# Performance work log

Measured on AMD Instinct MI355X. Metric: run time of the kernel, lower is better.

The kernel has to match this reference:

```python
import jax, jax.numpy as jnp
import numpy as np

B, H, W, T, D = 8, 32, 32, 4, 768
BLK = 4  # super-block of base tokens used to generate the static partition


def _build_descs():
    """Deterministic partition: 4x4 blocks of the 32x32 grid, scale = block_idx % 3."""
    d0, d1, d2 = [], [], []
    for t in range(T):
        i = 0
        for by in range(0, H, BLK):
            for bx in range(0, W, BLK):
                s = i % 3
                i += 1
                if s == 0:  # 16 base (scale-0) tokens
                    for yy in range(by, by + BLK):
                        for xx in range(bx, bx + BLK):
                            d0.append((yy, xx, t))
                elif s == 1:  # four 2x2 (scale-1) tokens
                    for yy in range(by, by + BLK, 2):
                        for xx in range(bx, bx + BLK, 2):
                            d1.append((yy, xx, t))
                else:  # one 4x4 (scale-2) token
                    d2.append((by, bx, t))
    return (jnp.asarray(np.array(d0, dtype=np.int32)),
            jnp.asarray(np.array(d1, dtype=np.int32)),
            jnp.asarray(np.array(d2, dtype=np.int32)))


def setup_inputs() -> dict:
    key = jax.random.key(0)
    ks = jax.random.split(key, 8)
    base = jax.random.normal(ks[0], (B, H, W, T, D), dtype=jnp.float32)
    desc0, desc1, desc2 = _build_descs()  # [1408,3], [336,3], [84,3] of (y, x, t)
    ws = 0.05  # keep conv outputs O(1)
    w1 = jax.random.normal(ks[1], (D, D, 2, 2), jnp.float32) * ws
    b1 = jax.random.normal(ks[2], (D,), jnp.float32) * ws
    w2a = jax.random.normal(ks[3], (D, D, 2, 2), jnp.float32) * ws
    b2a = jax.random.normal(ks[4], (D,), jnp.float32) * ws
    w2b = jax.random.normal(ks[5], (D, D, 2, 2), jnp.float32) * ws
    b2b = jax.random.normal(ks[6], (D,), jnp.float32) * ws
    return {"base_patch_embeddings": base, "desc0": desc0, "desc1": desc1,
            "desc2": desc2, "w1": w1, "b1": b1, "w2a": w2a, "b2a": b2a,
            "w2b": w2b, "b2b": b2b}


def _gather_blocks(base, desc, S):
    """Gather [B, N, S, S, D] blocks at (y, x, t) descriptors."""
    off = jnp.arange(S)
    ys = desc[:, 0][:, None, None] + off[None, :, None]  # [N,S,1]
    xs = desc[:, 1][:, None, None] + off[None, None, :]  # [N,1,S]
    ts = desc[:, 2][:, None, None]                       # [N,1,1]
    return base[:, ys, xs, ts, :]                        # [B,N,S,S,D]


def _down(x, w, b):
    """One k=2, s=2 conv over grouped blocks: [B,N,S,S,D] -> [B,N,S/2,S/2,D]."""
    Bn, N, S, _, Dd = x.shape
    x = x.reshape(Bn, N, S // 2, 2, S // 2, 2, Dd)
    return jnp.einsum('bnhiwjc,dcij->bnhwd', x, w) + b


def reference(base_patch_embeddings, desc0, desc1, desc2, w1, b1, w2a, b2a, w2b, b2b):
    base = base_patch_embeddings
    # scale 0: direct gather of base tokens
    tok0 = base[:, desc0[:, 0], desc0[:, 1], desc0[:, 2], :]          # [B,N0,D]
    # scale 1: 2x2 blocks -> one conv
    blk1 = _gather_blocks(base, desc1, 2)                             # [B,N1,2,2,D]
    tok1 = _down(blk1, w1, b1)[:, :, 0, 0, :]                         # [B,N1,D]
    # scale 2: 4x4 blocks -> two convs
    blk2 = _gather_blocks(base, desc2, 4)                             # [B,N2,4,4,D]
    tok2 = _down(_down(blk2, w2a, b2a), w2b, b2b)[:, :, 0, 0, :]      # [B,N2,D]
    tokens = jnp.concatenate([tok0, tok1, tok2], axis=1)              # [B,1828,D]
    # positions: (y, x, size_in_base, timestep)
    def _pos(desc, size):
        n = desc.shape[0]
        return jnp.concatenate([desc[:, :2],
                                jnp.full((n, 1), size, jnp.int32),
                                desc[:, 2:3]], axis=1)
    positions = jnp.concatenate([_pos(desc0, 1), _pos(desc1, 2), _pos(desc2, 4)], axis=0)
    return tokens, positions
```

## Files before the change

### kernel.cpp

```cpp
#include <hip/hip_runtime.h>
#include <cstdint>
#include <cstddef>

#define BB    8
#define HH    32
#define WW    32
#define TT    4
#define DD    768
#define N0    1408
#define N1    336
#define N2    84
#define NTOK  1828
#define TOK_FLOATS (BB*NTOK*DD)
#define KDIM  3072
#define M1    (BB*N1)
#define M2A   (BB*N2*4)
#define M2B   (BB*N2)

typedef __attribute__((ext_vector_type(8))) short          short8v;
typedef __attribute__((ext_vector_type(8))) unsigned short us8;
typedef __attribute__((ext_vector_type(4))) float          f32x4;

__device__ __forceinline__ unsigned short f2bf(float f) {
    unsigned int u = __float_as_uint(f);
    u += 0x7fffu + ((u >> 16) & 1u);
    return (unsigned short)(u >> 16);
}

__global__ __launch_bounds__(256) void positions_kernel(
    const int* __restrict__ d0, const int* __restrict__ d1,
    const int* __restrict__ d2, float* __restrict__ pos)
{
    int n = blockIdx.x * 256 + threadIdx.x;
    if (n >= NTOK) return;
    int y, x, t, s;
    if (n < N0)           { y = d0[n*3];         x = d0[n*3+1];         t = d0[n*3+2];         s = 1; }
    else if (n < N0+N1)   { int m = n - N0;      y = d1[m*3]; x = d1[m*3+1]; t = d1[m*3+2];    s = 2; }
    else                  { int m = n - N0 - N1; y = d2[m*3]; x = d2[m*3+1]; t = d2[m*3+2];    s = 4; }
    pos[n*4+0] = (float)y; pos[n*4+1] = (float)x; pos[n*4+2] = (float)s; pos[n*4+3] = (float)t;
}

__global__ __launch_bounds__(256) void gather0_kernel(
    const float* __restrict__ base, const int* __restrict__ d0,
    float* __restrict__ out)
{
    const int total = BB * N0 * (DD/4);
    for (int idx = blockIdx.x * 256 + threadIdx.x; idx < total; idx += gridDim.x * 256) {
        int d4 = idx % (DD/4);
        int nb = idx / (DD/4);
        int n  = nb % N0;
        int b  = nb / N0;
        int y = d0[n*3], x = d0[n*3+1], t = d0[n*3+2];
        const float4* src = (const float4*)(base + (size_t)(((b*HH + y)*WW + x)*TT + t) * DD) + d4;
        float4*       dst = (float4*)(out + ((size_t)b*NTOK + n) * DD) + d4;
        *dst = *src;
    }
}

__global__ __launch_bounds__(256) void castW_kernel(
    const float* __restrict__ wA, unsigned short* __restrict__ oA,
    const float* __restrict__ wB, unsigned short* __restrict__ oB,
    const float* __restrict__ wC, unsigned short* __restrict__ oC)
{
    const float* w; unsigned short* Wtb;
    if      (blockIdx.z == 0) { w = wA; Wtb = oA; }
    else if (blockIdx.z == 1) { w = wB; Wtb = oB; }
    else                      { w = wC; Wtb = oC; }
    int idx = blockIdx.x * 256 + threadIdx.x;
    int n = idx / KDIM;
    int r = idx - n * KDIM;
    int p = r / DD;
    int c = r - p * DD;
    Wtb[idx] = f2bf(w[n*KDIM + c*4 + p]);
}

__global__ __launch_bounds__(256) void gatherA_kernel(
    const float* __restrict__ base, const int* __restrict__ d1,
    const int* __restrict__ d2, unsigned short* __restrict__ A1,
    unsigned short* __restrict__ A2, int half)
{
    int idx = blockIdx.x * 256 + threadIdx.x;
    int rm = idx / 384;
    int o  = idx - rm * 384;
    if (half == 2) rm += M1;
    int k0 = o * 8;
    int p  = k0 / DD, c0 = k0 - p * DD;
    const float* rowp;
    unsigned short* dst;
    if (rm < M1) {
        int m = rm, b = m / N1, tok = m - b * N1;
        int y = d1[tok*3] + (p>>1), x = d1[tok*3+1] + (p&1), t = d1[tok*3+2];
        rowp = base + (size_t)(((b*HH + y)*WW + x)*TT + t) * DD;
        dst  = A1 + (size_t)m * KDIM + k0;
    } else {
        int m = rm - M1, b = m / (N2*4), r = m - b * (N2*4);
        int n = r >> 2, hw = r & 3, h = hw >> 1, w = hw & 1;
        int y = d2[n*3] + 2*h + (p>>1), x = d2[n*3+1] + 2*w + (p&1), t = d2[n*3+2];
        rowp = base + (size_t)(((b*HH + y)*WW + x)*TT + t) * DD;
        dst  = A2 + (size_t)m * KDIM + k0;
    }
    float4 v0 = *(const float4*)(rowp + c0);
    float4 v1 = *(const float4*)(rowp + c0 + 4);
    us8 r8;
    r8[0]=f2bf(v0.x); r8[1]=f2bf(v0.y); r8[2]=f2bf(v0.z); r8[3]=f2bf(v0.w);
    r8[4]=f2bf(v1.x); r8[5]=f2bf(v1.y); r8[6]=f2bf(v1.z); r8[7]=f2bf(v1.w);
    *(us8*)dst = r8;
}

struct GCfg {
    const unsigned short* A;
    const unsigned short* Bw;
    const float*          bias;
    float*                outf;
    unsigned short*       outb;
    int                   M;
    int                   mode;
};

__global__ __launch_bounds__(256) void mfma_gemm_kernel(GCfg c0, GCfg c1)
{
    GCfg cfg = (blockIdx.z == 0) ? c0 : c1;
    constexpr int LDT = 72;
    __shared__ unsigned short As[64  * LDT];
    __shared__ unsigned short Bs[128 * LDT];

    const int tid  = threadIdx.x;
    const int lane = tid & 63;
    const int wv   = tid >> 6;
    const int wr   = wv >> 1, wc = wv & 1;
    const int m0   = blockIdx.x * 64, n0 = blockIdx.y * 128;

    const int ar = tid >> 2, aci = (tid & 3) * 2;
    const int br = tid >> 1, bci = (tid & 1) * 4;
    int mrow = m0 + ar; if (mrow >= cfg.M) mrow = cfg.M - 1;
    const unsigned short* aptr = cfg.A  + (size_t)mrow    * KDIM + aci * 8;
    const unsigned short* bptr = cfg.Bw + (size_t)(n0+br) * KDIM + bci * 8;

    f32x4 acc[2][4];
    #pragma unroll
    for (int i = 0; i < 2; ++i)
        #pragma unroll
        for (int j = 0; j < 4; ++j)
            #pragma unroll
            for (int r = 0; r < 4; ++r) acc[i][j][r] = 0.f;

    us8 a0, a1, b0, b1, b2, b3;
    a0 = *(const us8*)(aptr);      a1 = *(const us8*)(aptr + 8);
    b0 = *(const us8*)(bptr);      b1 = *(const us8*)(bptr + 8);
    b2 = *(const us8*)(bptr + 16); b3 = *(const us8*)(bptr + 24);

    for (int k0 = 0; k0 < KDIM; k0 += 64) {
        __syncthreads();
        *(us8*)&As[ar*LDT +  aci   *8] = a0;
        *(us8*)&As[ar*LDT + (aci+1)*8] = a1;
        *(us8*)&Bs[br*LDT +  bci   *8] = b0;
        *(us8*)&Bs[br*LDT + (bci+1)*8] = b1;
        *(us8*)&Bs[br*LDT + (bci+2)*8] = b2;
        *(us8*)&Bs[br*LDT + (bci+3)*8] = b3;
        __syncthreads();
        if (k0 + 64 < KDIM) {
            const unsigned short* ap = aptr + k0 + 64;
            const unsigned short* bp = bptr + k0 + 64;
            a0 = *(const us8*)(ap);      a1 = *(const us8*)(ap + 8);
            b0 = *(const us8*)(bp);      b1 = *(const us8*)(bp + 8);
            b2 = *(const us8*)(bp + 16); b3 = *(const us8*)(bp + 24);
        }
        #pragma unroll
        for (int ks = 0; ks < 2; ++ks) {
            short8v av[2], bv[4];
            #pragma unroll
            for (int fm = 0; fm < 2; ++fm) {
                int row = wr*32 + fm*16 + (lane & 15);
                av[fm] = *(const short8v*)&As[row*LDT + (ks*4 + (lane>>4))*8];
            }
            #pragma unroll
            for (int fn = 0; fn < 4; ++fn) {
                int row = wc*64 + fn*16 + (lane & 15);
                bv[fn] = *(const short8v*)&Bs[row*LDT + (ks*4 + (lane>>4))*8];
            }
            #pragma unroll
            for (int fm = 0; fm < 2; ++fm)
                #pragma unroll
                for (int fn = 0; fn < 4; ++fn)
                    acc[fm][fn] = __builtin_amdgcn_mfma_f32_16x16x32_bf16(
                        av[fm], bv[fn], acc[fm][fn], 0, 0, 0);
        }
    }

    const int rg = lane >> 4, col = lane & 15;
    const int mode = cfg.mode;
    #pragma unroll
    for (int fm = 0; fm < 2; ++fm) {
        #pragma unroll
        for (int fn = 0; fn < 4; ++fn) {
            int n = n0 + wc*64 + fn*16 + col;
            float bs = cfg.bias[n];
            #pragma unroll
            for (int r = 0; r < 4; ++r) {
                int m = m0 + wr*32 + fm*16 + rg*4 + r;
                if (m >= cfg.M) continue;
                float v = acc[fm][fn][r] + bs;
                if (mode == 0) {
                    int b = m / N1, tok = m - b*N1;
                    cfg.outf[((size_t)b*NTOK + N0 + tok)*DD + n] = v;
                } else if (mode == 1) {
                    cfg.outb[(size_t)m*DD + n] = f2bf(v);
                } else {
                    int b = m / N2, tk = m - b*N2;
                    cfg.outf[((size_t)b*NTOK + N0 + N1 + tk)*DD + n] = v;
                }
            }
        }
    }
}

extern "C" void kernel_launch(void* const* d_in, const int* in_sizes, int n_in,
                              void* d_out, int out_size, void* d_ws, size_t ws_size,
                              hipStream_t stream)
{
    const float* base  = (const float*)d_in[0];
    const int*   desc0 = (const int*)  d_in[1];
    const int*   desc1 = (const int*)  d_in[2];
    const int*   desc2 = (const int*)  d_in[3];
    const float* w1    = (const float*)d_in[4];
    const float* b1    = (const float*)d_in[5];
    const float* w2a   = (const float*)d_in[6];
    const float* b2a   = (const float*)d_in[7];
    const float* w2b   = (const float*)d_in[8];
    const float* b2b   = (const float*)d_in[9];

    float* out = (float*)d_out;
    float* pos = (float*)d_out + TOK_FLOATS;
    unsigned short* ws = (unsigned short*)d_ws;

    positions_kernel<<<8, 256, 0, stream>>>(desc0, desc1, desc2, pos);
    gather0_kernel<<<2048, 256, 0, stream>>>(base, desc0, out);

    const size_t ABF = (size_t)M1 * KDIM;
    const size_t WTB = (size_t)DD * KDIM;
    const size_t Y1  = (size_t)M2A * DD;
    const size_t need_full = (2*ABF + Y1 + 3*WTB) * sizeof(unsigned short);

    if (ws_size >= need_full) {
        unsigned short* A1  = ws;
        unsigned short* A2  = A1  + ABF;
        unsigned short* y1b = A2  + ABF;
        unsigned short* W1  = y1b + Y1;
        unsigned short* W2a = W1  + WTB;
        unsigned short* W2b = W2a + WTB;
        castW_kernel<<<dim3(9216, 1, 3), 256, 0, stream>>>(w1, W1, w2a, W2a, w2b, W2b);
        gatherA_kernel<<<8064, 256, 0, stream>>>(base, desc1, desc2, A1, A2, 0);
        GCfg cA = { A1, W1,  b1,  out,     nullptr, M1,  0 };
        GCfg cB = { A2, W2a, b2a, nullptr, y1b,     M2A, 1 };
        mfma_gemm_kernel<<<dim3(42, 6, 2), 256, 0, stream>>>(cA, cB);
        GCfg cC = { y1b, W2b, b2b, out, nullptr, M2B, 2 };
        mfma_gemm_kernel<<<dim3(11, 6, 1), 256, 0, stream>>>(cC, cC);
    } else {
        unsigned short* A1  = ws;
        unsigned short* Wt  = A1 + ABF;
        unsigned short* y1b = Wt + WTB;
        castW_kernel<<<dim3(9216, 1, 1), 256, 0, stream>>>(w1, Wt, w1, Wt, w1, Wt);
        gatherA_kernel<<<4032, 256, 0, stream>>>(base, desc1, desc2, A1, A1, 1);
        GCfg cA = { A1, Wt, b1, out, nullptr, M1, 0 };
        mfma_gemm_kernel<<<dim3(42, 6, 1), 256, 0, stream>>>(cA, cA);
        castW_kernel<<<dim3(9216, 1, 1), 256, 0, stream>>>(w2a, Wt, w2a, Wt, w2a, Wt);
        gatherA_kernel<<<4032, 256, 0, stream>>>(base, desc1, desc2, A1, A1, 2);
        GCfg cB = { A1, Wt, b2a, nullptr, y1b, M2A, 1 };
        mfma_gemm_kernel<<<dim3(42, 6, 1), 256, 0, stream>>>(cB, cB);
        castW_kernel<<<dim3(9216, 1, 1), 256, 0, stream>>>(w2b, Wt, w2b, Wt, w2b, Wt);
        GCfg cC = { y1b, Wt, b2b, out, nullptr, M2B, 2 };
        mfma_gemm_kernel<<<dim3(11, 6, 1), 256, 0, stream>>>(cC, cC);
    }
}
```

Baseline: 320.7 us.

## Enlarge GEMM tiles to 128x128 with BK=96, XCD swizzle, vectorize weight cast

The MFMA GEMM moves from 64x128 tiles with 256 threads to 128x128 tiles with 512 threads and a K-step of 96. It uses a flattened 1D grid with an XCD-aware workgroup remap so that neighbouring tiles share L2. The weight cast kernel now reads float4 rows and scatters four bf16 values, cutting thread count and strided reads. Larger tiles mean fewer blocks (252 for the fused pair), which may underfill the GPU's CUs.

```diff
diff --git a/kernel.cpp b/kernel.cpp
--- a/kernel.cpp
+++ b/kernel.cpp
@@ -67,11 +67,11 @@
     else if (blockIdx.z == 1) { w = wB; Wtb = oB; }
     else                      { w = wC; Wtb = oC; }
     int idx = blockIdx.x * 256 + threadIdx.x;
-    int n = idx / KDIM;
-    int r = idx - n * KDIM;
-    int p = r / DD;
-    int c = r - p * DD;
-    Wtb[idx] = f2bf(w[n*KDIM + c*4 + p]);
+    int d = idx / DD;
+    int c = idx - d * DD;
+    float4 v = *(const float4*)(w + (size_t)d * KDIM + c * 4);
+    unsigned short* o = Wtb + (size_t)d * KDIM + c;
+    o[0*DD] = f2bf(v.x); o[1*DD] = f2bf(v.y); o[2*DD] = f2bf(v.z); o[3*DD] = f2bf(v.w);
 }
 
 __global__ __launch_bounds__(256) void gatherA_kernel(
@@ -117,87 +117,97 @@
     int                   mode;
 };
 
-__global__ __launch_bounds__(256) void mfma_gemm_kernel(GCfg c0, GCfg c1)
-{
-    GCfg cfg = (blockIdx.z == 0) ? c0 : c1;
-    constexpr int LDT = 72;
-    __shared__ unsigned short As[64  * LDT];
+__global__ __launch_bounds__(512) void mfma_gemm_kernel(
+    GCfg c0, GCfg c1, int nper, int mblks, int swz)
+{
+    constexpr int BK = 96, LDT = 104;
+    __shared__ unsigned short As[128 * LDT];
     __shared__ unsigned short Bs[128 * LDT];
+
+    int wgid = blockIdx.x;
+    if (swz) {
+        int nwg = gridDim.x;
+        int q = nwg >> 3, r = nwg & 7;
+        int xcd = wgid & 7, k = wgid >> 3;
+        wgid = (xcd < r ? xcd * (q + 1) : r * (q + 1) + (xcd - r) * q) + k;
+    }
+    GCfg cfg = c0;
+    if (wgid >= nper) { cfg = c1; wgid -= nper; }
+    const int nb = wgid / mblks, mb = wgid - nb * mblks;
+    const int m0 = mb * 128, n0 = nb * 128;
 
     const int tid  = threadIdx.x;
     const int lane = tid & 63;
     const int wv   = tid >> 6;
-    const int wr   = wv >> 1, wc = wv & 1;
-    const int m0   = blockIdx.x * 64, n0 = blockIdx.y * 128;
-
-    const int ar = tid >> 2, aci = (tid & 3) * 2;
-    const int br = tid >> 1, bci = (tid & 1) * 4;
+    const int wr   = wv >> 2, wc = wv & 3;
+    const int lr   = lane & 15, lq = lane >> 4;
+
+    const int ar = tid >> 2, ac = tid & 3;
     int mrow = m0 + ar; if (mrow >= cfg.M) mrow = cfg.M - 1;
-    const unsigned short* aptr = cfg.A  + (size_t)mrow    * KDIM + aci * 8;
-    const unsigned short* bptr = cfg.Bw + (size_t)(n0+br) * KDIM + bci * 8;
-
-    f32x4 acc[2][4];
+    const unsigned short* aptr = cfg.A  + (size_t)mrow     * KDIM;
+    const unsigned short* bptr = cfg.Bw + (size_t)(n0 + ar) * KDIM;
+
+    f32x4 acc[4][2];
     #pragma unroll
-    for (int i = 0; i < 2; ++i)
-        #pragma unroll
-        for (int j = 0; j < 4; ++j)
+    for (int i = 0; i < 4; ++i)
+        #pragma unroll
+        for (int j = 0; j < 2; ++j)
             #pragma unroll
             for (int r = 0; r < 4; ++r) acc[i][j][r] = 0.f;
 
-    us8 a0, a1, b0, b1, b2, b3;
-    a0 = *(const us8*)(aptr);      a1 = *(const us8*)(aptr + 8);
-    b0 = *(const us8*)(bptr);      b1 = *(const us8*)(bptr + 8);
-    b2 = *(const us8*)(bptr + 16); b3 = *(const us8*)(bptr + 24);
-
-    for (int k0 = 0; k0 < KDIM; k0 += 64) {
+    us8 areg[3], breg[3];
+    #pragma unroll
+    for (int k = 0; k < 3; ++k) {
+        int off = (ac + 4*k) * 8;
+        areg[k] = *(const us8*)(aptr + off);
+        breg[k] = *(const us8*)(bptr + off);
+    }
+
+    for (int k0 = 0; k0 < KDIM; k0 += BK) {
         __syncthreads();
-        *(us8*)&As[ar*LDT +  aci   *8] = a0;
-        *(us8*)&As[ar*LDT + (aci+1)*8] = a1;
-        *(us8*)&Bs[br*LDT +  bci   *8] = b0;
-        *(us8*)&Bs[br*LDT + (bci+1)*8] = b1;
-        *(us8*)&Bs[br*LDT + (bci+2)*8] = b2;
-        *(us8*)&Bs[br*LDT + (bci+3)*8] = b3;
+        #pragma unroll
+        for (int k = 0; k < 3; ++k) {
+            int o = ac + 4*k;
+            *(us8*)&As[ar*LDT + o*8] = areg[k];
+            *(us8*)&Bs[ar*LDT + o*8] = breg[k];
+        }
         __syncthreads();
-        if (k0 + 64 < KDIM) {
-            const unsigned short* ap = aptr + k0 + 64;
-            const unsigned short* bp = bptr + k0 + 64;
-            a0 = *(const us8*)(ap);      a1 = *(const us8*)(ap + 8);
-            b0 = *(const us8*)(bp);      b1 = *(const us8*)(bp + 8);
-            b2 = *(const us8*)(bp + 16); b3 = *(const us8*)(bp + 24);
-        }
-        #pragma unroll
-        for (int ks = 0; ks < 2; ++ks) {
-            short8v av[2], bv[4];
-            #pragma unroll
-            for (int fm = 0; fm < 2; ++fm) {
-                int row = wr*32 + fm*16 + (lane & 15);
-                av[fm] = *(const short8v*)&As[row*LDT + (ks*4 + (lane>>4))*8];
+        if (k0 + BK < KDIM) {
+            #pragma unroll
+            for (int k = 0; k < 3; ++k) {
+                int off = k0 + BK + (ac + 4*k) * 8;
+                areg[k] = *(const us8*)(aptr + off);
+                breg[k] = *(const us8*)(bptr + off);
             }
-            #pragma unroll
-            for (int fn = 0; fn < 4; ++fn) {
-                int row = wc*64 + fn*16 + (lane & 15);
-                bv[fn] = *(const short8v*)&Bs[row*LDT + (ks*4 + (lane>>4))*8];
-            }
-            #pragma unroll
-            for (int fm = 0; fm < 2; ++fm)
+        }
+        #pragma unroll
+        for (int ks = 0; ks < 3; ++ks) {
+            short8v av[4], bv[2];
+            #pragma unroll
+            for (int fm = 0; fm < 4; ++fm)
+                av[fm] = *(const short8v*)&As[(wr*64 + fm*16 + lr)*LDT + (ks*4 + lq)*8];
+            #pragma unroll
+            for (int fn = 0; fn < 2; ++fn)
+                bv[fn] = *(const short8v*)&Bs[(wc*32 + fn*16 + lr)*LDT + (ks*4 + lq)*8];
+            #pragma unroll
+            for (int fm = 0; fm < 4; ++fm)
                 #pragma unroll
-                for (int fn = 0; fn < 4; ++fn)
+                for (int fn = 0; fn < 2; ++fn)
                     acc[fm][fn] = __builtin_amdgcn_mfma_f32_16x16x32_bf16(
                         av[fm], bv[fn], acc[fm][fn], 0, 0, 0);
         }
     }
 
-    const int rg = lane >> 4, col = lane & 15;
     const int mode = cfg.mode;
     #pragma unroll
-    for (int fm = 0; fm < 2; ++fm) {
-        #pragma unroll
-        for (int fn = 0; fn < 4; ++fn) {
-            int n = n0 + wc*64 + fn*16 + col;
+    for (int fm = 0; fm < 4; ++fm) {
+        #pragma unroll
+        for (int fn = 0; fn < 2; ++fn) {
+            int n = n0 + wc*32 + fn*16 + lr;
             float bs = cfg.bias[n];
             #pragma unroll
             for (int r = 0; r < 4; ++r) {
-                int m = m0 + wr*32 + fm*16 + rg*4 + r;
+                int m = m0 + wr*64 + fm*16 + lq*4 + r;
                 if (m >= cfg.M) continue;
                 float v = acc[fm][fn][r] + bs;
                 if (mode == 0) {
@@ -248,27 +258,27 @@
         unsigned short* W1  = y1b + Y1;
         unsigned short* W2a = W1  + WTB;
         unsigned short* W2b = W2a + WTB;
-        castW_kernel<<<dim3(9216, 1, 3), 256, 0, stream>>>(w1, W1, w2a, W2a, w2b, W2b);
+        castW_kernel<<<dim3(2304, 1, 3), 256, 0, stream>>>(w1, W1, w2a, W2a, w2b, W2b);
         gatherA_kernel<<<8064, 256, 0, stream>>>(base, desc1, desc2, A1, A2, 0);
         GCfg cA = { A1, W1,  b1,  out,     nullptr, M1,  0 };
         GCfg cB = { A2, W2a, b2a, nullptr, y1b,     M2A, 1 };
-        mfma_gemm_kernel<<<dim3(42, 6, 2), 256, 0, stream>>>(cA, cB);
+        mfma_gemm_kernel<<<252, 512, 0, stream>>>(cA, cB, 126, 21, 1);
         GCfg cC = { y1b, W2b, b2b, out, nullptr, M2B, 2 };
-        mfma_gemm_kernel<<<dim3(11, 6, 1), 256, 0, stream>>>(cC, cC);
+        mfma_gemm_kernel<<<36, 512, 0, stream>>>(cC, cC, 36, 6, 0);
     } else {
         unsigned short* A1  = ws;
         unsigned short* Wt  = A1 + ABF;
         unsigned short* y1b = Wt + WTB;
-        castW_kernel<<<dim3(9216, 1, 1), 256, 0, stream>>>(w1, Wt, w1, Wt, w1, Wt);
+        castW_kernel<<<dim3(2304, 1, 1), 256, 0, stream>>>(w1, Wt, w1, Wt, w1, Wt);
         gatherA_kernel<<<4032, 256, 0, stream>>>(base, desc1, desc2, A1, A1, 1);
         GCfg cA = { A1, Wt, b1, out, nullptr, M1, 0 };
-        mfma_gemm_kernel<<<dim3(42, 6, 1), 256, 0, stream>>>(cA, cA);
-        castW_kernel<<<dim3(9216, 1, 1), 256, 0, stream>>>(w2a, Wt, w2a, Wt, w2a, Wt);
+        mfma_gemm_kernel<<<126, 512, 0, stream>>>(cA, cA, 126, 21, 1);
+        castW_kernel<<<dim3(2304, 1, 1), 256, 0, stream>>>(w2a, Wt, w2a, Wt, w2a, Wt);
         gatherA_kernel<<<4032, 256, 0, stream>>>(base, desc1, desc2, A1, A1, 2);
         GCfg cB = { A1, Wt, b2a, nullptr, y1b, M2A, 1 };
-        mfma_gemm_kernel<<<dim3(42, 6, 1), 256, 0, stream>>>(cB, cB);
-        castW_kernel<<<dim3(9216, 1, 1), 256, 0, stream>>>(w2b, Wt, w2b, Wt, w2b, Wt);
+        mfma_gemm_kernel<<<126, 512, 0, stream>>>(cB, cB, 126, 21, 1);
+        castW_kernel<<<dim3(2304, 1, 1), 256, 0, stream>>>(w2b, Wt, w2b, Wt, w2b, Wt);
         GCfg cC = { y1b, Wt, b2b, out, nullptr, M2B, 2 };
-        mfma_gemm_kernel<<<dim3(11, 6, 1), 256, 0, stream>>>(cC, cC);
-    }
-}
+        mfma_gemm_kernel<<<36, 512, 0, stream>>>(cC, cC, 36, 6, 0);
+    }
+}
```

Result: faster. 305.9 us (-4.6%).

## Fuse prep kernels and double-buffer GEMM with direct global-to-LDS swizzled loads

Applied to the files above, without the earlier changes.

Merges the positions, scale-0 gather, weight cast and A-gather kernels into one prep launch, which cuts launch overhead. The GEMM now stages tiles through global_load_lds into double-buffered LDS, using an XOR swizzle that is pre-applied to A, the weights and the intermediate y1 so LDS reads avoid bank conflicts. Workgroup IDs are remapped so each XCD gets a share of blocks. The weight cast is rewritten to read float4 coalesced, and the small-workspace fallback path is dropped.

```diff
diff --git a/kernel.cpp b/kernel.cpp
--- a/kernel.cpp
+++ b/kernel.cpp
@@ -27,84 +27,87 @@
     return (unsigned short)(u >> 16);
 }
 
-__global__ __launch_bounds__(256) void positions_kernel(
-    const int* __restrict__ d0, const int* __restrict__ d1,
-    const int* __restrict__ d2, float* __restrict__ pos)
+__device__ __forceinline__ void cp16(const unsigned short* g, unsigned short* l) {
+    __builtin_amdgcn_global_load_lds(
+        (const __attribute__((address_space(1))) unsigned int*)(const void*)g,
+        (__attribute__((address_space(3))) unsigned int*)(void*)l,
+        16, 0, 0);
+}
+
+#define GA_BLKS 8064
+#define CW_BLKS 6912
+#define G0_BLKS 2048
+#define PREP_BLKS (GA_BLKS + CW_BLKS + G0_BLKS + 8)
+
+__global__ __launch_bounds__(256) void prep_kernel(
+    const float* __restrict__ base, const int* __restrict__ d0,
+    const int* __restrict__ d1, const int* __restrict__ d2,
+    const float* __restrict__ w1, const float* __restrict__ w2a,
+    const float* __restrict__ w2b,
+    unsigned short* __restrict__ A1, unsigned short* __restrict__ A2,
+    unsigned short* __restrict__ W1, unsigned short* __restrict__ W2a,
+    unsigned short* __restrict__ W2b,
+    float* __restrict__ out, float* __restrict__ pos)
 {
-    int n = blockIdx.x * 256 + threadIdx.x;
-    if (n >= NTOK) return;
-    int y, x, t, s;
-    if (n < N0)           { y = d0[n*3];         x = d0[n*3+1];         t = d0[n*3+2];         s = 1; }
-    else if (n < N0+N1)   { int m = n - N0;      y = d1[m*3]; x = d1[m*3+1]; t = d1[m*3+2];    s = 2; }
-    else                  { int m = n - N0 - N1; y = d2[m*3]; x = d2[m*3+1]; t = d2[m*3+2];    s = 4; }
-    pos[n*4+0] = (float)y; pos[n*4+1] = (float)x; pos[n*4+2] = (float)s; pos[n*4+3] = (float)t;
-}
-
-__global__ __launch_bounds__(256) void gather0_kernel(
-    const float* __restrict__ base, const int* __restrict__ d0,
-    float* __restrict__ out)
-{
-    const int total = BB * N0 * (DD/4);
-    for (int idx = blockIdx.x * 256 + threadIdx.x; idx < total; idx += gridDim.x * 256) {
-        int d4 = idx % (DD/4);
-        int nb = idx / (DD/4);
-        int n  = nb % N0;
-        int b  = nb / N0;
-        int y = d0[n*3], x = d0[n*3+1], t = d0[n*3+2];
-        const float4* src = (const float4*)(base + (size_t)(((b*HH + y)*WW + x)*TT + t) * DD) + d4;
-        float4*       dst = (float4*)(out + ((size_t)b*NTOK + n) * DD) + d4;
-        *dst = *src;
+    const int blk = blockIdx.x, tid = threadIdx.x;
+    if (blk < GA_BLKS) {
+        int idx = blk * 256 + tid;
+        int rm = idx / 384, o = idx - rm * 384;
+        int s = (o & ~7) | ((o ^ rm) & 7);
+        int p = s / 96, c0 = (s - p * 96) * 8;
+        const float* rowp;
+        unsigned short* dst;
+        if (rm < M1) {
+            int m = rm, b = m / N1, tok = m - b * N1;
+            int y = d1[tok*3] + (p>>1), x = d1[tok*3+1] + (p&1), t = d1[tok*3+2];
+            rowp = base + (size_t)(((b*HH + y)*WW + x)*TT + t) * DD;
+            dst  = A1 + (size_t)m * KDIM + o * 8;
+        } else {
+            int m = rm - M1, b = m / (N2*4), r = m - b * (N2*4);
+            int n = r >> 2, hw = r & 3, h = hw >> 1, w = hw & 1;
+            int y = d2[n*3] + 2*h + (p>>1), x = d2[n*3+1] + 2*w + (p&1), t = d2[n*3+2];
+            rowp = base + (size_t)(((b*HH + y)*WW + x)*TT + t) * DD;
+            dst  = A2 + (size_t)m * KDIM + o * 8;
+        }
+        float4 v0 = *(const float4*)(rowp + c0);
+        float4 v1 = *(const float4*)(rowp + c0 + 4);
+        us8 r8;
+        r8[0]=f2bf(v0.x); r8[1]=f2bf(v0.y); r8[2]=f2bf(v0.z); r8[3]=f2bf(v0.w);
+        r8[4]=f2bf(v1.x); r8[5]=f2bf(v1.y); r8[6]=f2bf(v1.z); r8[7]=f2bf(v1.w);
+        *(us8*)dst = r8;
+    } else if (blk < GA_BLKS + CW_BLKS) {
+        int r = blk - GA_BLKS;
+        int wsel = r / 2304;
+        int idx  = (r - wsel * 2304) * 256 + tid;
+        const float* w        = wsel==0 ? w1 : (wsel==1 ? w2a : w2b);
+        unsigned short* Wt    = wsel==0 ? W1 : (wsel==1 ? W2a : W2b);
+        int d = idx / DD, c = idx - d * DD;
+        float4 v = *(const float4*)(w + (size_t)d * KDIM + c * 4);
+        int csw = (c & ~63) | ((((c>>3) ^ d) & 7) << 3) | (c & 7);
+        unsigned short* o = Wt + (size_t)d * KDIM + csw;
+        o[0*DD] = f2bf(v.x); o[1*DD] = f2bf(v.y); o[2*DD] = f2bf(v.z); o[3*DD] = f2bf(v.w);
+    } else if (blk < GA_BLKS + CW_BLKS + G0_BLKS) {
+        int bl = blk - GA_BLKS - CW_BLKS;
+        const int total = BB * N0 * (DD/4);
+        for (int idx = bl * 256 + tid; idx < total; idx += G0_BLKS * 256) {
+            int d4 = idx % (DD/4);
+            int nb = idx / (DD/4);
+            int n  = nb % N0;
+            int b  = nb / N0;
+            int y = d0[n*3], x = d0[n*3+1], t = d0[n*3+2];
+            const float4* src = (const float4*)(base + (size_t)(((b*HH + y)*WW + x)*TT + t) * DD) + d4;
+            float4*       dst = (float4*)(out + ((size_t)b*NTOK + n) * DD) + d4;
+            *dst = *src;
+        }
+    } else {
+        int n = (blk - GA_BLKS - CW_BLKS - G0_BLKS) * 256 + tid;
+        if (n >= NTOK) return;
+        int y, x, t, s;
+        if (n < N0)         { y = d0[n*3];         x = d0[n*3+1];         t = d0[n*3+2];       s = 1; }
+        else if (n < N0+N1) { int m = n - N0;      y = d1[m*3]; x = d1[m*3+1]; t = d1[m*3+2];  s = 2; }
+        else                { int m = n - N0 - N1; y = d2[m*3]; x = d2[m*3+1]; t = d2[m*3+2];  s = 4; }
+        pos[n*4+0] = (float)y; pos[n*4+1] = (float)x; pos[n*4+2] = (float)s; pos[n*4+3] = (float)t;
     }
-}
-
-__global__ __launch_bounds__(256) void castW_kernel(
-    const float* __restrict__ wA, unsigned short* __restrict__ oA,
-    const float* __restrict__ wB, unsigned short* __restrict__ oB,
-    const float* __restrict__ wC, unsigned short* __restrict__ oC)
-{
-    const float* w; unsigned short* Wtb;
-    if      (blockIdx.z == 0) { w = wA; Wtb = oA; }
-    else if (blockIdx.z == 1) { w = wB; Wtb = oB; }
-    else                      { w = wC; Wtb = oC; }
-    int idx = blockIdx.x * 256 + threadIdx.x;
-    int n = idx / KDIM;
-    int r = idx - n * KDIM;
-    int p = r / DD;
-    int c = r - p * DD;
-    Wtb[idx] = f2bf(w[n*KDIM + c*4 + p]);
-}
-
-__global__ __launch_bounds__(256) void gatherA_kernel(
-    const float* __restrict__ base, const int* __restrict__ d1,
-    const int* __restrict__ d2, unsigned short* __restrict__ A1,
-    unsigned short* __restrict__ A2, int half)
-{
-    int idx = blockIdx.x * 256 + threadIdx.x;
-    int rm = idx / 384;
-    int o  = idx - rm * 384;
-    if (half == 2) rm += M1;
-    int k0 = o * 8;
-    int p  = k0 / DD, c0 = k0 - p * DD;
-    const float* rowp;
-    unsigned short* dst;
-    if (rm < M1) {
-        int m = rm, b = m / N1, tok = m - b * N1;
-        int y = d1[tok*3] + (p>>1), x = d1[tok*3+1] + (p&1), t = d1[tok*3+2];
-        rowp = base + (size_t)(((b*HH + y)*WW + x)*TT + t) * DD;
-        dst  = A1 + (size_t)m * KDIM + k0;
-    } else {
-        int m = rm - M1, b = m / (N2*4), r = m - b * (N2*4);
-        int n = r >> 2, hw = r & 3, h = hw >> 1, w = hw & 1;
-        int y = d2[n*3] + 2*h + (p>>1), x = d2[n*3+1] + 2*w + (p&1), t = d2[n*3+2];
-        rowp = base + (size_t)(((b*HH + y)*WW + x)*TT + t) * DD;
-        dst  = A2 + (size_t)m * KDIM + k0;
-    }
-    float4 v0 = *(const float4*)(rowp + c0);
-    float4 v1 = *(const float4*)(rowp + c0 + 4);
-    us8 r8;
-    r8[0]=f2bf(v0.x); r8[1]=f2bf(v0.y); r8[2]=f2bf(v0.z); r8[3]=f2bf(v0.w);
-    r8[4]=f2bf(v1.x); r8[5]=f2bf(v1.y); r8[6]=f2bf(v1.z); r8[7]=f2bf(v1.w);
-    *(us8*)dst = r8;
 }
 
 struct GCfg {
@@ -117,24 +120,34 @@
     int                   mode;
 };
 
-__global__ __launch_bounds__(256) void mfma_gemm_kernel(GCfg c0, GCfg c1)
+__global__ __launch_bounds__(256) void mfma_gemm_v3(
+    GCfg c0, GCfg c1, int nper, int mblks, int swz)
 {
-    GCfg cfg = (blockIdx.z == 0) ? c0 : c1;
-    constexpr int LDT = 72;
-    __shared__ unsigned short As[64  * LDT];
-    __shared__ unsigned short Bs[128 * LDT];
-
-    const int tid  = threadIdx.x;
-    const int lane = tid & 63;
-    const int wv   = tid >> 6;
-    const int wr   = wv >> 1, wc = wv & 1;
-    const int m0   = blockIdx.x * 64, n0 = blockIdx.y * 128;
-
-    const int ar = tid >> 2, aci = (tid & 3) * 2;
-    const int br = tid >> 1, bci = (tid & 1) * 4;
-    int mrow = m0 + ar; if (mrow >= cfg.M) mrow = cfg.M - 1;
-    const unsigned short* aptr = cfg.A  + (size_t)mrow    * KDIM + aci * 8;
-    const unsigned short* bptr = cfg.Bw + (size_t)(n0+br) * KDIM + bci * 8;
+    __shared__ unsigned short As[2][64 * 64];
+    __shared__ unsigned short Bs[2][128 * 64];
+
+    int wgid = blockIdx.x;
+    if (swz) wgid = (wgid & 7) * (gridDim.x >> 3) + (wgid >> 3);
+    GCfg cfg = c0;
+    if (wgid >= nper) { cfg = c1; wgid -= nper; }
+    const int nb = wgid / mblks, mb = wgid - nb * mblks;
+    const int m0 = mb * 64, n0 = nb * 128;
+
+    const int tid = threadIdx.x, lane = tid & 63;
+    const int wv = tid >> 6, wr = wv >> 1, wc = wv & 1;
+    const int lr = lane & 15, lq = lane >> 4, xr = lr & 7;
+
+    const int aoct = tid & 7, trow = tid >> 3;
+    int am0 = m0 + trow;      if (am0 >= cfg.M) am0 = cfg.M - 1;
+    int am1 = m0 + 32 + trow; if (am1 >= cfg.M) am1 = cfg.M - 1;
+    const unsigned short* ag0 = cfg.A + (size_t)am0 * KDIM + aoct * 8;
+    const unsigned short* ag1 = cfg.A + (size_t)am1 * KDIM + aoct * 8;
+    const unsigned short* bg0 = cfg.Bw + (size_t)(n0 +      trow) * KDIM + aoct * 8;
+    const unsigned short* bg1 = cfg.Bw + (size_t)(n0 + 32 + trow) * KDIM + aoct * 8;
+    const unsigned short* bg2 = cfg.Bw + (size_t)(n0 + 64 + trow) * KDIM + aoct * 8;
+    const unsigned short* bg3 = cfg.Bw + (size_t)(n0 + 96 + trow) * KDIM + aoct * 8;
+
+    const int wu = tid & 192;
 
     f32x4 acc[2][4];
     #pragma unroll
@@ -144,39 +157,40 @@
             #pragma unroll
             for (int r = 0; r < 4; ++r) acc[i][j][r] = 0.f;
 
-    us8 a0, a1, b0, b1, b2, b3;
-    a0 = *(const us8*)(aptr);      a1 = *(const us8*)(aptr + 8);
-    b0 = *(const us8*)(bptr);      b1 = *(const us8*)(bptr + 8);
-    b2 = *(const us8*)(bptr + 16); b3 = *(const us8*)(bptr + 24);
-
-    for (int k0 = 0; k0 < KDIM; k0 += 64) {
-        __syncthreads();
-        *(us8*)&As[ar*LDT +  aci   *8] = a0;
-        *(us8*)&As[ar*LDT + (aci+1)*8] = a1;
-        *(us8*)&Bs[br*LDT +  bci   *8] = b0;
-        *(us8*)&Bs[br*LDT + (bci+1)*8] = b1;
-        *(us8*)&Bs[br*LDT + (bci+2)*8] = b2;
-        *(us8*)&Bs[br*LDT + (bci+3)*8] = b3;
-        __syncthreads();
-        if (k0 + 64 < KDIM) {
-            const unsigned short* ap = aptr + k0 + 64;
-            const unsigned short* bp = bptr + k0 + 64;
-            a0 = *(const us8*)(ap);      a1 = *(const us8*)(ap + 8);
-            b0 = *(const us8*)(bp);      b1 = *(const us8*)(bp + 8);
-            b2 = *(const us8*)(bp + 16); b3 = *(const us8*)(bp + 24);
-        }
+    auto STAGE = [&](int buf, int k0) {
+        cp16(ag0 + k0, &As[buf][(0*256 + wu) * 8]);
+        cp16(ag1 + k0, &As[buf][(1*256 + wu) * 8]);
+        cp16(bg0 + k0, &Bs[buf][(0*256 + wu) * 8]);
+        cp16(bg1 + k0, &Bs[buf][(1*256 + wu) * 8]);
+        cp16(bg2 + k0, &Bs[buf][(2*256 + wu) * 8]);
+        cp16(bg3 + k0, &Bs[buf][(3*256 + wu) * 8]);
+    };
+
+    STAGE(0, 0);
+    constexpr int NIT = KDIM / 64;
+    for (int it = 0; it < NIT; ++it) {
+        const int cur = it & 1;
+        if (it + 1 < NIT) {
+            STAGE(cur ^ 1, (it + 1) * 64);
+            asm volatile("s_waitcnt vmcnt(6)" ::: "memory");
+        } else {
+            asm volatile("s_waitcnt vmcnt(0)" ::: "memory");
+        }
+        __builtin_amdgcn_s_barrier();
+        const unsigned short* Asb = As[cur];
+        const unsigned short* Bsb = Bs[cur];
         #pragma unroll
         for (int ks = 0; ks < 2; ++ks) {
             short8v av[2], bv[4];
             #pragma unroll
             for (int fm = 0; fm < 2; ++fm) {
-                int row = wr*32 + fm*16 + (lane & 15);
-                av[fm] = *(const short8v*)&As[row*LDT + (ks*4 + (lane>>4))*8];
+                int row = wr*32 + fm*16 + lr;
+                av[fm] = *(const short8v*)&Asb[row*64 + ((ks*4 + lq) ^ xr) * 8];
             }
             #pragma unroll
             for (int fn = 0; fn < 4; ++fn) {
-                int row = wc*64 + fn*16 + (lane & 15);
-                bv[fn] = *(const short8v*)&Bs[row*LDT + (ks*4 + (lane>>4))*8];
+                int row = wc*64 + fn*16 + lr;
+                bv[fn] = *(const short8v*)&Bsb[row*64 + ((ks*4 + lq) ^ xr) * 8];
             }
             #pragma unroll
             for (int fm = 0; fm < 2; ++fm)
@@ -185,26 +199,27 @@
                     acc[fm][fn] = __builtin_amdgcn_mfma_f32_16x16x32_bf16(
                         av[fm], bv[fn], acc[fm][fn], 0, 0, 0);
         }
+        __builtin_amdgcn_s_barrier();
     }
 
-    const int rg = lane >> 4, col = lane & 15;
     const int mode = cfg.mode;
     #pragma unroll
     for (int fm = 0; fm < 2; ++fm) {
         #pragma unroll
         for (int fn = 0; fn < 4; ++fn) {
-            int n = n0 + wc*64 + fn*16 + col;
+            int n = n0 + wc*64 + fn*16 + lr;
             float bs = cfg.bias[n];
             #pragma unroll
             for (int r = 0; r < 4; ++r) {
-                int m = m0 + wr*32 + fm*16 + rg*4 + r;
+                int m = m0 + wr*32 + fm*16 + lq*4 + r;
                 if (m >= cfg.M) continue;
                 float v = acc[fm][fn][r] + bs;
                 if (mode == 0) {
                     int b = m / N1, tok = m - b*N1;
                     cfg.outf[((size_t)b*NTOK + N0 + tok)*DD + n] = v;
                 } else if (mode == 1) {
-                    cfg.outb[(size_t)m*DD + n] = f2bf(v);
+                    int nsw = (n & ~63) | ((((n>>3) ^ (m>>2)) & 7) << 3) | (n & 7);
+                    cfg.outb[(size_t)m*DD + nsw] = f2bf(v);
                 } else {
                     int b = m / N2, tk = m - b*N2;
                     cfg.outf[((size_t)b*NTOK + N0 + N1 + tk)*DD + n] = v;
@@ -233,42 +248,24 @@
     float* pos = (float*)d_out + TOK_FLOATS;
     unsigned short* ws = (unsigned short*)d_ws;
 
-    positions_kernel<<<8, 256, 0, stream>>>(desc0, desc1, desc2, pos);
-    gather0_kernel<<<2048, 256, 0, stream>>>(base, desc0, out);
-
     const size_t ABF = (size_t)M1 * KDIM;
+    const size_t Y1  = (size_t)M2A * DD;
     const size_t WTB = (size_t)DD * KDIM;
-    const size_t Y1  = (size_t)M2A * DD;
-    const size_t need_full = (2*ABF + Y1 + 3*WTB) * sizeof(unsigned short);
-
-    if (ws_size >= need_full) {
-        unsigned short* A1  = ws;
-        unsigned short* A2  = A1  + ABF;
-        unsigned short* y1b = A2  + ABF;
-        unsigned short* W1  = y1b + Y1;
-        unsigned short* W2a = W1  + WTB;
-        unsigned short* W2b = W2a + WTB;
-        castW_kernel<<<dim3(9216, 1, 3), 256, 0, stream>>>(w1, W1, w2a, W2a, w2b, W2b);
-        gatherA_kernel<<<8064, 256, 0, stream>>>(base, desc1, desc2, A1, A2, 0);
-        GCfg cA = { A1, W1,  b1,  out,     nullptr, M1,  0 };
-        GCfg cB = { A2, W2a, b2a, nullptr, y1b,     M2A, 1 };
-        mfma_gemm_kernel<<<dim3(42, 6, 2), 256, 0, stream>>>(cA, cB);
-        GCfg cC = { y1b, W2b, b2b, out, nullptr, M2B, 2 };
-        mfma_gemm_kernel<<<dim3(11, 6, 1), 256, 0, stream>>>(cC, cC);
-    } else {
-        unsigned short* A1  = ws;
-        unsigned short* Wt  = A1 + ABF;
-        unsigned short* y1b = Wt + WTB;
-        castW_kernel<<<dim3(9216, 1, 1), 256, 0, stream>>>(w1, Wt, w1, Wt, w1, Wt);
-        gatherA_kernel<<<4032, 256, 0, stream>>>(base, desc1, desc2, A1, A1, 1);
-        GCfg cA = { A1, Wt, b1, out, nullptr, M1, 0 };
-        mfma_gemm_kernel<<<dim3(42, 6, 1), 256, 0, stream>>>(cA, cA);
-        castW_kernel<<<dim3(9216, 1, 1), 256, 0, stream>>>(w2a, Wt, w2a, Wt, w2a, Wt);
-        gatherA_kernel<<<4032, 256, 0, stream>>>(base, desc1, desc2, A1, A1, 2);
-        GCfg cB = { A1, Wt, b2a, nullptr, y1b, M2A, 1 };
-        mfma_gemm_kernel<<<dim3(42, 6, 1), 256, 0, stream>>>(cB, cB);
-        castW_kernel<<<dim3(9216, 1, 1), 256, 0, stream>>>(w2b, Wt, w2b, Wt, w2b, Wt);
-        GCfg cC = { y1b, Wt, b2b, out, nullptr, M2B, 2 };
-        mfma_gemm_kernel<<<dim3(11, 6, 1), 256, 0, stream>>>(cC, cC);
-    }
-}
+    unsigned short* A1  = ws;
+    unsigned short* A2  = A1  + ABF;
+    unsigned short* y1b = A2  + ABF;
+    unsigned short* W1  = y1b + Y1;
+    unsigned short* W2a = W1  + WTB;
+    unsigned short* W2b = W2a + WTB;
+
+    prep_kernel<<<PREP_BLKS, 256, 0, stream>>>(
+        base, desc0, desc1, desc2, w1, w2a, w2b,
+        A1, A2, W1, W2a, W2b, out, pos);
+
+    GCfg cA = { A1, W1,  b1,  out,     nullptr, M1,  0 };
+    GCfg cB = { A2, W2a, b2a, nullptr, y1b,     M2A, 1 };
+    mfma_gemm_v3<<<504, 256, 0, stream>>>(cA, cB, 252, 42, 1);
+
+    GCfg cC = { y1b, W2b, b2b, out, nullptr, M2B, 2 };
+    mfma_gemm_v3<<<66, 256, 0, stream>>>(cC, cC, 66, 11, 0);
+}
```

After: 296.4 us. 1.08x faster.
